# Kernel tuning notes

Hardware: AMD Instinct MI355X
Metric: run time of the kernel (lower is better)

## Reference

```python
import jax, jax.numpy as jnp
import numpy as np

N_NODES = 10000
N_EDGES = 160000
MUL = 16  # multiplicity of each irrep in irreps_in/out: '16x0e + 16x1o'
DIM_IN = 4 * MUL  # 16 scalars + 16 vectors*3 = 64
FC_HIDDEN = 256
WEIGHT_NUMEL = 4 * MUL * MUL  # 4 CG paths, uvw weights (16,1,16) each


def setup_inputs() -> dict:
    key = jax.random.key(0)
    ks = jax.random.split(key, 7)
    return {
        "edge_src": jax.random.randint(ks[0], (N_EDGES,), 0, N_NODES),
        "edge_dst": jax.random.randint(ks[1], (N_EDGES,), 0, N_NODES),
        "node_features": jax.random.normal(ks[2], (N_NODES, DIM_IN), jnp.float32),
        "edge_sh": jax.random.normal(ks[3], (N_EDGES, 4), jnp.float32),
        "edge_length_embedded": jax.random.uniform(ks[4], (N_EDGES, 3), dtype=jnp.float32),
        "fc_w1": jax.random.normal(ks[5], (3, FC_HIDDEN), jnp.float32),
        "fc_w2": jax.random.normal(ks[6], (FC_HIDDEN, WEIGHT_NUMEL), jnp.float32),
        "num_neighbors": 16,
    }


def _fc_net(x, w1, w2):
    # e3nn FullyConnectedNet([3,256,weight_numel], relu): no bias,
    # weights scaled by 1/sqrt(fan_in), relu normalized to unit 2nd moment (*sqrt(2)).
    h = jax.nn.relu(x @ (w1 / np.sqrt(3.0))) * np.sqrt(2.0)
    return h @ (w2 / np.sqrt(float(FC_HIDDEN)))


def _forward(edge_src, edge_dst, node_features, edge_sh, edge_length_embedded,
             fc_w1, fc_w2, num_neighbors):
    E = edge_sh.shape[0]
    w = _fc_net(edge_length_embedded, fc_w1, fc_w2).reshape(E, 4, MUL, MUL)  # per-edge TP weights

    x = node_features[edge_src]                 # gather: [E, 64]
    s0 = x[:, :MUL]                             # [E,16]  0e scalars
    v1 = x[:, MUL:].reshape(E, MUL, 3)          # [E,16,3] 1o vectors
    y0 = edge_sh[:, 0:1]                        # [E,1]   sh 0e
    y1 = edge_sh[:, 1:4]                        # [E,3]   sh 1o

    inv_sqrt3 = 1.0 / np.sqrt(3.0)              # w3j(0,1,1), w3j(1,0,1), w3j(1,1,0) = delta/sqrt(3)
    # path_weight: irrep_normalization='component' (alpha = 2l_out+1),
    # path_normalization='element' (fan_in per output irrep = 16+16 = 32)
    pw0 = np.sqrt(1.0 / 32.0)                   # 0e output
    pw1 = np.sqrt(3.0 / 32.0)                   # 1o output

    # 0e output: (0e x 0e -> 0e) + (1o x 1o -> 0e)
    out0 = pw0 * (jnp.einsum('eu,euw->ew', s0 * y0, w[:, 0])
                  + inv_sqrt3 * jnp.einsum('eui,ei,euw->ew', v1, y1, w[:, 1]))
    # 1o output: (0e x 1o -> 1o) + (1o x 0e -> 1o)
    out1 = pw1 * inv_sqrt3 * (jnp.einsum('eu,ei,euw->ewi', s0, y1, w[:, 2])
                              + jnp.einsum('eui,euw->ewi', v1 * y0[:, :, None], w[:, 3]))

    edge_features = jnp.concatenate([out0, out1.reshape(E, 3 * MUL)], axis=1)  # [E,64]
    out = jax.ops.segment_sum(edge_features, edge_dst, num_segments=N_NODES)   # scatter-add
    return out / np.sqrt(float(num_neighbors))


def reference(edge_src, edge_dst, node_features, edge_sh, edge_length_embedded,
              fc_w1, fc_w2, num_neighbors):
    return _forward(edge_src, edge_dst, node_features, edge_sh, edge_length_embedded,
                    fc_w1, fc_w2, num_neighbors)
```

## Files before the change

### kernel.cpp

```cpp
#include <hip/hip_runtime.h>
#include <hip/hip_bf16.h>

#define N_NODES 10000
#define N_EDGES 160000
#define TE 64

typedef __attribute__((ext_vector_type(8))) short bfrag_t;
typedef __attribute__((ext_vector_type(4))) float facc_t;

__device__ inline short f2bf(float f) {
    union { float f; unsigned u; } x; x.f = f;
    unsigned r = x.u + 0x7FFFu + ((x.u >> 16) & 1u);
    return (short)(r >> 16);
}

__global__ void pack_w2(const float* __restrict__ w2, short* __restrict__ outp) {
    int g = blockIdx.x * blockDim.x + threadIdx.x;
    int j    = g & 7;
    int lane = (g >> 3) & 63;
    int k    = (g >> 9) & 7;
    int nt   = (g >> 12) & 15;
    int p    = g >> 16;
    int row = k * 32 + ((lane >> 4) << 3) + j;
    int col = p * 256 + nt * 16 + (lane & 15);
    outp[g] = f2bf(w2[row * 1024 + col] * 0.0625f);
}

__global__ void zero_counts(int* __restrict__ counts) {
    int i = blockIdx.x * blockDim.x + threadIdx.x;
    if (i < N_NODES) counts[i] = 0;
}

__global__ void hist_kernel(const int* __restrict__ edst, int* __restrict__ counts) {
    int e = blockIdx.x * blockDim.x + threadIdx.x;
    if (e < N_EDGES) atomicAdd(&counts[edst[e]], 1);
}

__global__ __launch_bounds__(256) void scan_kernel(const int* __restrict__ counts,
                                                   int* __restrict__ cursor) {
    __shared__ int part[256];
    const int t = threadIdx.x;
    const int CH = 40;
    int base = t * CH;
    int s = 0;
    for (int i = 0; i < CH; ++i) {
        int idx = base + i;
        if (idx < N_NODES) s += counts[idx];
    }
    part[t] = s;
    __syncthreads();
    for (int off = 1; off < 256; off <<= 1) {
        int add = (t >= off) ? part[t - off] : 0;
        __syncthreads();
        part[t] += add;
        __syncthreads();
    }
    int run = part[t] - s;
    for (int i = 0; i < CH; ++i) {
        int idx = base + i;
        if (idx < N_NODES) {
            cursor[idx] = run;
            run += counts[idx];
        }
    }
}

__global__ void scatter_kernel(const int* __restrict__ edst, int* __restrict__ cursor,
                               int* __restrict__ perm) {
    int e = blockIdx.x * blockDim.x + threadIdx.x;
    if (e < N_EDGES) {
        int pos = atomicAdd(&cursor[edst[e]], 1);
        perm[pos] = e;
    }
}

__global__ __launch_bounds__(512) void conv_kernel(
    const int* __restrict__ perm,
    const int* __restrict__ esrc, const int* __restrict__ edst,
    const float* __restrict__ nodef, const float* __restrict__ esh,
    const float* __restrict__ ell, const float* __restrict__ w1,
    const short* __restrict__ w2p, const int* __restrict__ nn,
    float* __restrict__ outg)
{
    __shared__ __align__(16) char hbuf[TE * 512];
    short* h_lds  = (short*)hbuf;
    float* r0_lds = (float*)hbuf;
    float* r1_lds = (float*)(hbuf + 4352);
    float* r2_lds = (float*)(hbuf + 8704);
    float* r3_lds = (float*)(hbuf + 13056);
    __shared__ __align__(16) float x_lds[TE][68];
    float* vbuf = (float*)x_lds;
    __shared__ float a0_lds[TE][17];
    __shared__ float a1_lds[TE][17];
    __shared__ float sh_lds[TE][4];
    __shared__ float el_lds[TE][3];
    __shared__ int   src_lds[TE];
    __shared__ int   dst_lds[TE];
    __shared__ int   head_lds[TE];

    const int tid = threadIdx.x;
    const int e0  = blockIdx.x * TE;

    if (tid < TE) {
        int pe = perm[e0 + tid];
        src_lds[tid] = esrc[pe];
        dst_lds[tid] = edst[pe];
        float4 s4 = *(const float4*)(esh + (size_t)pe * 4);
        sh_lds[tid][0] = s4.x; sh_lds[tid][1] = s4.y;
        sh_lds[tid][2] = s4.z; sh_lds[tid][3] = s4.w;
        const float* lp = ell + (size_t)pe * 3;
        el_lds[tid][0] = lp[0]; el_lds[tid][1] = lp[1]; el_lds[tid][2] = lp[2];
    }
    __syncthreads();

    {
        int e = tid >> 3, part = tid & 7;
        int s = src_lds[e];
        const float4* sp = (const float4*)(nodef + (size_t)s * 64 + part * 8);
        float4 u0 = sp[0], u1 = sp[1];
        float* xr = &x_lds[e][part * 8];
        *(float4*)(xr)     = u0;
        *(float4*)(xr + 4) = u1;
    }
    {
        int e = tid >> 3, c0 = (tid & 7) * 32;
        float l0 = el_lds[e][0], l1 = el_lds[e][1], l2 = el_lds[e][2];
        #pragma unroll
        for (int s = 0; s < 4; ++s) {
            bfrag_t hv;
            #pragma unroll
            for (int m = 0; m < 8; ++m) {
                int c = c0 + s * 8 + m;
                float a = l0 * w1[c] + l1 * w1[256 + c] + l2 * w1[512 + c];
                a = fmaxf(a, 0.f) * 0.8164965809277260f;
                hv[m] = f2bf(a);
            }
            int byte = (e * 512 + (c0 + s * 8) * 2) ^ ((e & 7) << 4);
            *(bfrag_t*)((char*)h_lds + byte) = hv;
        }
    }
    __syncthreads();
    {
        #pragma unroll
        for (int q = tid; q < TE * 16; q += 512) {
            int e = q >> 4, u = q & 15;
            float y0 = sh_lds[e][0];
            a0_lds[e][u] = x_lds[e][u] * y0;
            a1_lds[e][u] = x_lds[e][16 + u * 3 + 0] * sh_lds[e][1]
                         + x_lds[e][16 + u * 3 + 1] * sh_lds[e][2]
                         + x_lds[e][16 + u * 3 + 2] * sh_lds[e][3];
        }
    }
    __syncthreads();

    const int lane = tid & 63;
    const int wv   = tid >> 6;
    const int p    = wv & 3;
    const int mh   = wv >> 2;
    const int g    = lane >> 4;
    const int v    = lane & 15;
    const int eb   = 32 * mh;

    float acc0[2][4];
    float acc3[2][4][3];
    #pragma unroll
    for (int mt = 0; mt < 2; ++mt)
        #pragma unroll
        for (int r = 0; r < 4; ++r) {
            acc0[mt][r] = 0.f;
            acc3[mt][r][0] = 0.f; acc3[mt][r][1] = 0.f; acc3[mt][r][2] = 0.f;
        }

    const bfrag_t* Bp = (const bfrag_t*)w2p + (size_t)(p * 128) * 64 + lane;

    const int rb0 = (eb + v) * 512;
    const int rb1 = (eb + 16 + v) * 512;
    const int swz = (v & 7) << 4;

    #pragma unroll
    for (int ntc = 0; ntc < 4; ++ntc) {
        facc_t acc[2][4];
        #pragma unroll
        for (int mt = 0; mt < 2; ++mt)
            #pragma unroll
            for (int q = 0; q < 4; ++q)
                acc[mt][q] = (facc_t){0.f, 0.f, 0.f, 0.f};

        #pragma unroll
        for (int k = 0; k < 8; ++k) {
            int koff = (k * 32 + 8 * g) * 2;
            bfrag_t a0 = *(const bfrag_t*)((const char*)h_lds + ((rb0 + koff) ^ swz));
            bfrag_t a1 = *(const bfrag_t*)((const char*)h_lds + ((rb1 + koff) ^ swz));
            #pragma unroll
            for (int q = 0; q < 4; ++q) {
                bfrag_t b = Bp[(size_t)((ntc * 4 + q) * 8 + k) * 64];
                acc[0][q] = __builtin_amdgcn_mfma_f32_16x16x32_bf16(a0, b, acc[0][q], 0, 0, 0);
                acc[1][q] = __builtin_amdgcn_mfma_f32_16x16x32_bf16(a1, b, acc[1][q], 0, 0, 0);
            }
        }
        #pragma unroll
        for (int mt = 0; mt < 2; ++mt)
            #pragma unroll
            for (int r = 0; r < 4; ++r) {
                int e = eb + mt * 16 + 4 * g + r;
                #pragma unroll
                for (int q = 0; q < 4; ++q) {
                    int u = ntc * 4 + q;
                    float wvl = acc[mt][q][r];
                    if (p == 0)       acc0[mt][r] += a0_lds[e][u] * wvl;
                    else if (p == 1)  acc0[mt][r] += a1_lds[e][u] * wvl;
                    else if (p == 2)  acc0[mt][r] += x_lds[e][u] * wvl;
                    else {
                        acc3[mt][r][0] += x_lds[e][16 + u * 3 + 0] * wvl;
                        acc3[mt][r][1] += x_lds[e][16 + u * 3 + 1] * wvl;
                        acc3[mt][r][2] += x_lds[e][16 + u * 3 + 2] * wvl;
                    }
                }
            }
    }

    __syncthreads();

    #pragma unroll
    for (int mt = 0; mt < 2; ++mt)
        #pragma unroll
        for (int r = 0; r < 4; ++r) {
            int e = eb + mt * 16 + 4 * g + r;
            if (p == 0)       r0_lds[e * 17 + v] = acc0[mt][r];
            else if (p == 1)  r1_lds[e * 17 + v] = acc0[mt][r];
            else if (p == 2)  r2_lds[e * 17 + v] = acc0[mt][r];
            else {
                r3_lds[e * 49 + v * 3 + 0] = acc3[mt][r][0];
                r3_lds[e * 49 + v * 3 + 1] = acc3[mt][r][1];
                r3_lds[e * 49 + v * 3 + 2] = acc3[mt][r][2];
            }
        }
    __syncthreads();

    {
        float scale = rsqrtf((float)nn[0]);
        const float pw0 = 0.17677669529663687f;
        float k0 = pw0 * scale;
        float k1 = k0 * 0.57735026918962576f;

        int e  = tid >> 3;
        int j0 = (tid & 7) * 8;
        float y0  = sh_lds[e][0];
        float y1x = sh_lds[e][1], y1y = sh_lds[e][2], y1z = sh_lds[e][3];
        #pragma unroll
        for (int jj = 0; jj < 8; ++jj) {
            int j = j0 + jj;
            float val;
            if (j < 16) {
                val = k0 * r0_lds[e * 17 + j] + k1 * r1_lds[e * 17 + j];
            } else {
                int t2 = j - 16;
                int vv = t2 / 3;
                int i  = t2 - vv * 3;
                float y1i = (i == 0) ? y1x : ((i == 1) ? y1y : y1z);
                val = k0 * (y1i * r2_lds[e * 17 + vv] + y0 * r3_lds[e * 49 + t2]);
            }
            vbuf[e * 68 + j] = val;
        }
    }
    if (tid < TE)
        head_lds[tid] = (tid == 0) || (dst_lds[tid] != dst_lds[tid - 1]);
    __syncthreads();
    {
        int e   = tid >> 3;
        int oct = tid & 7;
        if (head_lds[e]) {
            int L = 1;
            while (e + L < TE && !head_lds[e + L]) ++L;
            float4 s0 = *(const float4*)(vbuf + e * 68 + oct * 8);
            float4 s1 = *(const float4*)(vbuf + e * 68 + oct * 8 + 4);
            for (int i = 1; i < L; ++i) {
                const float4* q = (const float4*)(vbuf + (e + i) * 68 + oct * 8);
                float4 t0 = q[0], t1 = q[1];
                s0.x += t0.x; s0.y += t0.y; s0.z += t0.z; s0.w += t0.w;
                s1.x += t1.x; s1.y += t1.y; s1.z += t1.z; s1.w += t1.w;
            }
            float* op = outg + (size_t)dst_lds[e] * 64 + oct * 8;
            atomicAdd(op + 0, s0.x); atomicAdd(op + 1, s0.y);
            atomicAdd(op + 2, s0.z); atomicAdd(op + 3, s0.w);
            atomicAdd(op + 4, s1.x); atomicAdd(op + 5, s1.y);
            atomicAdd(op + 6, s1.z); atomicAdd(op + 7, s1.w);
        }
    }
}

extern "C" void kernel_launch(void* const* d_in, const int* in_sizes, int n_in,
                              void* d_out, int out_size, void* d_ws, size_t ws_size,
                              hipStream_t stream) {
    const int*   esrc  = (const int*)d_in[0];
    const int*   edst  = (const int*)d_in[1];
    const float* nodef = (const float*)d_in[2];
    const float* esh   = (const float*)d_in[3];
    const float* ellv  = (const float*)d_in[4];
    const float* w1    = (const float*)d_in[5];
    const float* w2    = (const float*)d_in[6];
    const int*   nn    = (const int*)d_in[7];
    float* outg = (float*)d_out;

    char* ws = (char*)d_ws;
    short* w2p    = (short*)ws;
    int*   counts = (int*)(ws + (512 << 10));
    int*   cursor = (int*)(ws + (512 << 10) + 65536);
    int*   permv  = (int*)(ws + (512 << 10) + 131072);

    hipMemsetAsync(d_out, 0, (size_t)out_size * sizeof(float), stream);
    pack_w2<<<1024, 256, 0, stream>>>(w2, w2p);
    zero_counts<<<(N_NODES + 255) / 256, 256, 0, stream>>>(counts);
    hist_kernel<<<N_EDGES / 256, 256, 0, stream>>>(edst, counts);
    scan_kernel<<<1, 256, 0, stream>>>(counts, cursor);
    scatter_kernel<<<N_EDGES / 256, 256, 0, stream>>>(edst, cursor, permv);
    conv_kernel<<<N_EDGES / TE, 512, 0, stream>>>(permv, esrc, edst, nodef, esh, ellv,
                                                  w1, w2p, nn, outg);
}
```

Before: 357.5 us.

## Split fused conv kernel into prep kernel and GEMM kernel via workspace

Adds a prep kernel that applies the edge permutation, gathers src/dst/sh, computes the first FC layer with ReLU and writes the hidden activations to global memory as swizzled bf16. A second GEMM kernel then loads those precomputed tiles straight into LDS and runs the MFMA tensor-product and segmented scatter. The aim is to take the FC1 and permutation gather work off the heavy kernel's critical path and cut its register and latency pressure. In exchange it writes and rereads about 80 MB of hidden activations and adds a launch, and it falls back to the old kernel when the workspace is too small.

After: 378.1 us. 5.8% more time.

```diff
diff --git a/kernel.cpp b/kernel.cpp
--- a/kernel.cpp
+++ b/kernel.cpp
@@ -3,6 +3,7 @@
 
 #define N_NODES 10000
 #define N_EDGES 160000
+#define TE1 32
 #define TE 64
 
 typedef __attribute__((ext_vector_type(8))) short bfrag_t;
@@ -71,6 +72,250 @@
     if (e < N_EDGES) {
         int pos = atomicAdd(&cursor[edst[e]], 1);
         perm[pos] = e;
+    }
+}
+
+__global__ __launch_bounds__(256) void prep_kernel(
+    const int* __restrict__ perm,
+    const int* __restrict__ esrc, const int* __restrict__ edst,
+    const float* __restrict__ esh, const float* __restrict__ ell,
+    const float* __restrict__ w1,
+    int* __restrict__ gsrc, int* __restrict__ gdst, float* __restrict__ gsh,
+    short* __restrict__ hg)
+{
+    __shared__ float el_lds[TE1][3];
+    const int tid = threadIdx.x;
+    const int e0  = blockIdx.x * TE1;
+
+    if (tid < TE1) {
+        int pe = perm[e0 + tid];
+        gsrc[e0 + tid] = esrc[pe];
+        gdst[e0 + tid] = edst[pe];
+        float4 s4 = *(const float4*)(esh + (size_t)pe * 4);
+        *(float4*)(gsh + (size_t)(e0 + tid) * 4) = s4;
+        const float* lp = ell + (size_t)pe * 3;
+        el_lds[tid][0] = lp[0]; el_lds[tid][1] = lp[1]; el_lds[tid][2] = lp[2];
+    }
+    __syncthreads();
+
+    {
+        int el = tid >> 3, c0 = (tid & 7) * 32;
+        int eg = e0 + el;
+        float l0 = el_lds[el][0], l1 = el_lds[el][1], l2 = el_lds[el][2];
+        #pragma unroll
+        for (int s = 0; s < 4; ++s) {
+            bfrag_t hv;
+            #pragma unroll
+            for (int m = 0; m < 8; ++m) {
+                int c = c0 + s * 8 + m;
+                float a = l0 * w1[c] + l1 * w1[256 + c] + l2 * w1[512 + c];
+                a = fmaxf(a, 0.f) * 0.8164965809277260f;
+                hv[m] = f2bf(a);
+            }
+            size_t byte = (size_t)eg * 512 + (((c0 + s * 8) * 2) ^ ((eg & 7) << 4));
+            *(bfrag_t*)((char*)hg + byte) = hv;
+        }
+    }
+}
+
+__global__ __launch_bounds__(512) void gemm_kernel(
+    const int* __restrict__ gsrc, const int* __restrict__ gdst,
+    const float* __restrict__ gsh, const short* __restrict__ hg,
+    const float* __restrict__ nodef,
+    const short* __restrict__ w2p, const int* __restrict__ nn,
+    float* __restrict__ outg)
+{
+    __shared__ __align__(16) char hbuf[TE * 512];
+    short* h_lds  = (short*)hbuf;
+    float* r0_lds = (float*)hbuf;
+    float* r1_lds = (float*)(hbuf + 4352);
+    float* r2_lds = (float*)(hbuf + 8704);
+    float* r3_lds = (float*)(hbuf + 13056);
+    __shared__ __align__(16) float x_lds[TE][68];
+    float* vbuf = (float*)x_lds;
+    __shared__ float a0_lds[TE][17];
+    __shared__ float a1_lds[TE][17];
+    __shared__ float sh_lds[TE][4];
+    __shared__ int   src_lds[TE];
+    __shared__ int   dst_lds[TE];
+    __shared__ int   head_lds[TE];
+
+    const int tid = threadIdx.x;
+    const int e0  = blockIdx.x * TE;
+
+    if (tid < TE) {
+        src_lds[tid] = gsrc[e0 + tid];
+        dst_lds[tid] = gdst[e0 + tid];
+        float4 s4 = *(const float4*)(gsh + (size_t)(e0 + tid) * 4);
+        sh_lds[tid][0] = s4.x; sh_lds[tid][1] = s4.y;
+        sh_lds[tid][2] = s4.z; sh_lds[tid][3] = s4.w;
+    }
+    __syncthreads();
+
+    {
+        int e = tid >> 3, part = tid & 7;
+        int s = src_lds[e];
+        const float4* sp = (const float4*)(nodef + (size_t)s * 64 + part * 8);
+        float4 u0 = sp[0], u1 = sp[1];
+        float* xr = &x_lds[e][part * 8];
+        *(float4*)(xr)     = u0;
+        *(float4*)(xr + 4) = u1;
+    }
+    {
+        const char* src = (const char*)hg + (size_t)e0 * 512;
+        #pragma unroll
+        for (int i = 0; i < 4; ++i) {
+            int byte = tid * 64 + i * 16;
+            *(float4*)(hbuf + byte) = *(const float4*)(src + byte);
+        }
+    }
+    __syncthreads();
+    {
+        #pragma unroll
+        for (int q = tid; q < TE * 16; q += 512) {
+            int e = q >> 4, u = q & 15;
+            float y0 = sh_lds[e][0];
+            a0_lds[e][u] = x_lds[e][u] * y0;
+            a1_lds[e][u] = x_lds[e][16 + u * 3 + 0] * sh_lds[e][1]
+                         + x_lds[e][16 + u * 3 + 1] * sh_lds[e][2]
+                         + x_lds[e][16 + u * 3 + 2] * sh_lds[e][3];
+        }
+    }
+    __syncthreads();
+
+    const int lane = tid & 63;
+    const int wv   = tid >> 6;
+    const int p    = wv & 3;
+    const int mh   = wv >> 2;
+    const int g    = lane >> 4;
+    const int v    = lane & 15;
+    const int eb   = 32 * mh;
+
+    float acc0[2][4];
+    float acc3[2][4][3];
+    #pragma unroll
+    for (int mt = 0; mt < 2; ++mt)
+        #pragma unroll
+        for (int r = 0; r < 4; ++r) {
+            acc0[mt][r] = 0.f;
+            acc3[mt][r][0] = 0.f; acc3[mt][r][1] = 0.f; acc3[mt][r][2] = 0.f;
+        }
+
+    const bfrag_t* Bp = (const bfrag_t*)w2p + (size_t)(p * 128) * 64 + lane;
+
+    const int rb0 = (eb + v) * 512;
+    const int rb1 = (eb + 16 + v) * 512;
+    const int swz = (v & 7) << 4;
+
+    #pragma unroll
+    for (int ntc = 0; ntc < 4; ++ntc) {
+        facc_t acc[2][4];
+        #pragma unroll
+        for (int mt = 0; mt < 2; ++mt)
+            #pragma unroll
+            for (int q = 0; q < 4; ++q)
+                acc[mt][q] = (facc_t){0.f, 0.f, 0.f, 0.f};
+
+        #pragma unroll
+        for (int k = 0; k < 8; ++k) {
+            int koff = (k * 32 + 8 * g) * 2;
+            bfrag_t a0 = *(const bfrag_t*)((const char*)h_lds + ((rb0 + koff) ^ swz));
+            bfrag_t a1 = *(const bfrag_t*)((const char*)h_lds + ((rb1 + koff) ^ swz));
+            #pragma unroll
+            for (int q = 0; q < 4; ++q) {
+                bfrag_t b = Bp[(size_t)((ntc * 4 + q) * 8 + k) * 64];
+                acc[0][q] = __builtin_amdgcn_mfma_f32_16x16x32_bf16(a0, b, acc[0][q], 0, 0, 0);
+                acc[1][q] = __builtin_amdgcn_mfma_f32_16x16x32_bf16(a1, b, acc[1][q], 0, 0, 0);
+            }
+        }
+        #pragma unroll
+        for (int mt = 0; mt < 2; ++mt)
+            #pragma unroll
+            for (int r = 0; r < 4; ++r) {
+                int e = eb + mt * 16 + 4 * g + r;
+                #pragma unroll
+                for (int q = 0; q < 4; ++q) {
+                    int u = ntc * 4 + q;
+                    float wvl = acc[mt][q][r];
+                    if (p == 0)       acc0[mt][r] += a0_lds[e][u] * wvl;
+                    else if (p == 1)  acc0[mt][r] += a1_lds[e][u] * wvl;
+                    else if (p == 2)  acc0[mt][r] += x_lds[e][u] * wvl;
+                    else {
+                        acc3[mt][r][0] += x_lds[e][16 + u * 3 + 0] * wvl;
+                        acc3[mt][r][1] += x_lds[e][16 + u * 3 + 1] * wvl;
+                        acc3[mt][r][2] += x_lds[e][16 + u * 3 + 2] * wvl;
+                    }
+                }
+            }
+    }
+
+    __syncthreads();
+
+    #pragma unroll
+    for (int mt = 0; mt < 2; ++mt)
+        #pragma unroll
+        for (int r = 0; r < 4; ++r) {
+            int e = eb + mt * 16 + 4 * g + r;
+            if (p == 0)       r0_lds[e * 17 + v] = acc0[mt][r];
+            else if (p == 1)  r1_lds[e * 17 + v] = acc0[mt][r];
+            else if (p == 2)  r2_lds[e * 17 + v] = acc0[mt][r];
+            else {
+                r3_lds[e * 49 + v * 3 + 0] = acc3[mt][r][0];
+                r3_lds[e * 49 + v * 3 + 1] = acc3[mt][r][1];
+                r3_lds[e * 49 + v * 3 + 2] = acc3[mt][r][2];
+            }
+        }
+    __syncthreads();
+
+    {
+        float scale = rsqrtf((float)nn[0]);
+        const float pw0 = 0.17677669529663687f;
+        float k0 = pw0 * scale;
+        float k1 = k0 * 0.57735026918962576f;
+
+        int e  = tid >> 3;
+        int j0 = (tid & 7) * 8;
+        float y0  = sh_lds[e][0];
+        float y1x = sh_lds[e][1], y1y = sh_lds[e][2], y1z = sh_lds[e][3];
+        #pragma unroll
+        for (int jj = 0; jj < 8; ++jj) {
+            int j = j0 + jj;
+            float val;
+            if (j < 16) {
+                val = k0 * r0_lds[e * 17 + j] + k1 * r1_lds[e * 17 + j];
+            } else {
+                int t2 = j - 16;
+                int vv = t2 / 3;
+                int i  = t2 - vv * 3;
+                float y1i = (i == 0) ? y1x : ((i == 1) ? y1y : y1z);
+                val = k0 * (y1i * r2_lds[e * 17 + vv] + y0 * r3_lds[e * 49 + t2]);
+            }
+            vbuf[e * 68 + j] = val;
+        }
+    }
+    if (tid < TE)
+        head_lds[tid] = (tid == 0) || (dst_lds[tid] != dst_lds[tid - 1]);
+    __syncthreads();
+    {
+        int e   = tid >> 3;
+        int oct = tid & 7;
+        if (head_lds[e]) {
+            int L = 1;
+            while (e + L < TE && !head_lds[e + L]) ++L;
+            float4 s0 = *(const float4*)(vbuf + e * 68 + oct * 8);
+            float4 s1 = *(const float4*)(vbuf + e * 68 + oct * 8 + 4);
+            for (int i = 1; i < L; ++i) {
+                const float4* q = (const float4*)(vbuf + (e + i) * 68 + oct * 8);
+                float4 t0 = q[0], t1 = q[1];
+                s0.x += t0.x; s0.y += t0.y; s0.z += t0.z; s0.w += t0.w;
+                s1.x += t1.x; s1.y += t1.y; s1.z += t1.z; s1.w += t1.w;
+            }
+            float* op = outg + (size_t)dst_lds[e] * 64 + oct * 8;
+            atomicAdd(op + 0, s0.x); atomicAdd(op + 1, s0.y);
+            atomicAdd(op + 2, s0.z); atomicAdd(op + 3, s0.w);
+            atomicAdd(op + 4, s1.x); atomicAdd(op + 5, s1.y);
+            atomicAdd(op + 6, s1.z); atomicAdd(op + 7, s1.w);
+        }
     }
 }
 
@@ -172,7 +417,6 @@
         }
 
     const bfrag_t* Bp = (const bfrag_t*)w2p + (size_t)(p * 128) * 64 + lane;
-
     const int rb0 = (eb + v) * 512;
     const int rb1 = (eb + 16 + v) * 512;
     const int swz = (v & 7) << 4;
@@ -303,10 +547,22 @@
     float* outg = (float*)d_out;
 
     char* ws = (char*)d_ws;
-    short* w2p    = (short*)ws;
-    int*   counts = (int*)(ws + (512 << 10));
-    int*   cursor = (int*)(ws + (512 << 10) + 65536);
-    int*   permv  = (int*)(ws + (512 << 10) + 131072);
+    size_t off = 0;
+    auto alloc = [&](size_t sz) { size_t r = off; off = (off + sz + 4095) & ~(size_t)4095; return r; };
+    size_t o_w2p  = alloc(524288);
+    size_t o_cnt  = alloc(40960);
+    size_t o_cur  = alloc(40960);
+    size_t o_perm = alloc((size_t)N_EDGES * 4);
+    size_t o_gsrc = alloc((size_t)N_EDGES * 4);
+    size_t o_gdst = alloc((size_t)N_EDGES * 4);
+    size_t o_gsh  = alloc((size_t)N_EDGES * 16);
+    size_t o_hg   = alloc((size_t)N_EDGES * 512);
+    int use_split = (ws_size >= off);
+
+    short* w2p    = (short*)(ws + o_w2p);
+    int*   counts = (int*)(ws + o_cnt);
+    int*   cursor = (int*)(ws + o_cur);
+    int*   permv  = (int*)(ws + o_perm);
 
     hipMemsetAsync(d_out, 0, (size_t)out_size * sizeof(float), stream);
     pack_w2<<<1024, 256, 0, stream>>>(w2, w2p);
@@ -314,6 +570,18 @@
     hist_kernel<<<N_EDGES / 256, 256, 0, stream>>>(edst, counts);
     scan_kernel<<<1, 256, 0, stream>>>(counts, cursor);
     scatter_kernel<<<N_EDGES / 256, 256, 0, stream>>>(edst, cursor, permv);
-    conv_kernel<<<N_EDGES / TE, 512, 0, stream>>>(permv, esrc, edst, nodef, esh, ellv,
-                                                  w1, w2p, nn, outg);
-}
+
+    if (use_split) {
+        int*   gsrc = (int*)(ws + o_gsrc);
+        int*   gdst = (int*)(ws + o_gdst);
+        float* gsh  = (float*)(ws + o_gsh);
+        short* hg   = (short*)(ws + o_hg);
+        prep_kernel<<<N_EDGES / TE1, 256, 0, stream>>>(permv, esrc, edst, esh, ellv, w1,
+                                                       gsrc, gdst, gsh, hg);
+        gemm_kernel<<<N_EDGES / TE, 512, 0, stream>>>(gsrc, gdst, gsh, hg, nodef,
+                                                      w2p, nn, outg);
+    } else {
+        conv_kernel<<<N_EDGES / TE, 512, 0, stream>>>(permv, esrc, edst, nodef, esh, ellv,
+                                                      w1, w2p, nn, outg);
+    }
+}
```
